# Kernel optimization log

Measured on AMD Instinct MI355X. Metric: run time of the kernel, lower is better.

Reference implementation:

```python
import jax, jax.numpy as jnp
import numpy as np

B, D_IN, D_H, D_OUT = 1024, 1024, 4096, 1024
SPARSITY = 0.5  # fraction of weights KEPT (top-k)


def setup_inputs() -> dict:
    key = jax.random.key(0)
    ks = jax.random.split(key, 13)
    def kaiming(k, shape):
        fan_in = shape[-1] if len(shape) > 1 else shape[0]
        bound = 1.0 / np.sqrt(fan_in)
        return jax.random.uniform(k, shape, jnp.float32, -bound, bound)
    inp = {
        "x":   jax.random.normal(ks[0], (B, D_IN), jnp.float32),
        "W1":  kaiming(ks[1], (D_H, D_IN)),
        "b1":  kaiming(ks[2], (D_H,)),
        "W2":  kaiming(ks[3], (D_H, D_H)),
        "b2":  kaiming(ks[4], (D_H,)),
        "W3":  kaiming(ks[5], (D_OUT, D_H)),
        "b3":  kaiming(ks[6], (D_OUT,)),
        # scores: kaiming-uniform for weights, N(0, 0.01) for biases (as in Mask.__init__)
        "sW1": kaiming(ks[7], (D_H, D_IN)),
        "sb1": 0.01 * jax.random.normal(ks[8], (D_H,), jnp.float32),
        "sW2": kaiming(ks[9], (D_H, D_H)),
        "sb2": 0.01 * jax.random.normal(ks[10], (D_H,), jnp.float32),
        "sW3": kaiming(ks[11], (D_OUT, D_H)),
        "sb3": 0.01 * jax.random.normal(ks[12], (D_OUT,), jnp.float32),
    }
    return inp


def _global_masks(scores):
    """Single fused global top-k threshold mask (replaces O(P) redundant sorts).
    Bottom (1-SPARSITY) fraction (by value rank) -> 0, top SPARSITY fraction -> 1."""
    flat = jnp.concatenate([s.ravel() for s in scores])
    n = flat.shape[0]
    j = int((1.0 - SPARSITY) * n)  # number of zeroed entries
    idx = jnp.argsort(flat)
    bin_mask = jnp.zeros((n,), flat.dtype).at[idx[j:]].set(1.0)
    # straight-through: d(mask)/d(score) = 1 (GetSubnet_global.backward returns g)
    st_mask = bin_mask + flat - jax.lax.stop_gradient(flat)
    sizes = [int(np.prod(s.shape)) for s in scores]
    offs = np.concatenate([[0], np.cumsum(sizes)])
    return [st_mask[offs[i]:offs[i + 1]].reshape(scores[i].shape)
            for i in range(len(scores))]


def reference(x, W1, b1, W2, b2, W3, b3, sW1, sb1, sW2, sb2, sW3, sb3):
    masks = _global_masks([sW1, sb1, sW2, sb2, sW3, sb3])
    mW1, mb1, mW2, mb2, mW3, mb3 = masks
    # masked params, then MLP forward (torch Linear: y = x @ W.T + b)
    h = jax.nn.relu(x @ (W1 * mW1).T + b1 * mb1)
    h = jax.nn.relu(h @ (W2 * mW2).T + b2 * mb2)
    return h @ (W3 * mW3).T + b3 * mb3
```

## Files before the change

### kernel.cpp

```cpp
#include <hip/hip_runtime.h>
#include <hip/hip_bf16.h>
#include <stdint.h>


typedef __bf16 bf16_t;
typedef __bf16 bf16x4 __attribute__((ext_vector_type(4)));
typedef __bf16 bf16x8 __attribute__((ext_vector_type(8)));
typedef float  f32x4  __attribute__((ext_vector_type(4)));

using gvoid = const __attribute__((address_space(1))) void;
using svoid = __attribute__((address_space(3))) void;

#define O1 4194304L
#define O2 4198400L
#define O3 20975616L
#define O4 20979712L
#define O5 25174016L
#define N_TOT 25175040L
#define J_RANK 12587520u
#define CAND_CAP 4096

#define HIST_BLOCKS 512

#define WS_HIST 0u
#define WS_RES  32768u
#define WS_CNT  32784u
#define WS_CAND 32800u
#define WS_W1B  131072u
#define WS_B1F  8519680u
#define WS_W2B  8536064u
#define WS_B2F  42090496u
#define WS_W3B  42106880u
#define WS_B3F  50495488u
#define WS_H1F  50511872u
#define WS_H2F  58900480u
#define WS_FAST_END 67289088ull
#define WS_H1   131072u
#define WS_H2   8519680u

#define SWZ(row, chunk) ((((chunk) + ((row) >> 1)) & 3))

__device__ __forceinline__ unsigned int mono32(float f) {
    unsigned int u = __float_as_uint(f);
    return (u & 0x80000000u) ? ~u : (u | 0x80000000u);
}

__global__ __launch_bounds__(256) void zero_kernel(unsigned int* p, int n) {
    int i = blockIdx.x * 256 + threadIdx.x;
    if (i < n) p[i] = 0u;
}

__global__ __launch_bounds__(256) void cvt_x_kernel(const float* __restrict__ x,
                                                    bf16_t* __restrict__ xb, int n8) {
    int i = blockIdx.x * 256 + threadIdx.x;
    if (i < n8) {
        const float4 a = *(const float4*)(x + (size_t)i * 8);
        const float4 b = *(const float4*)(x + (size_t)i * 8 + 4);
        bf16x8 r;
        r[0] = (__bf16)a.x; r[1] = (__bf16)a.y; r[2] = (__bf16)a.z; r[3] = (__bf16)a.w;
        r[4] = (__bf16)b.x; r[5] = (__bf16)b.y; r[6] = (__bf16)b.z; r[7] = (__bf16)b.w;
        *(bf16x8*)(xb + (size_t)i * 8) = r;
    }
}

__device__ __forceinline__ void seg_lookup(long e,
    const float* s0, const float* s1, const float* s2,
    const float* s3, const float* s4, const float* s5,
    const float** sp, long* off) {
    if (e < O1)      { *sp = s0; *off = e; }
    else if (e < O2) { *sp = s1; *off = e - O1; }
    else if (e < O3) { *sp = s2; *off = e - O2; }
    else if (e < O4) { *sp = s3; *off = e - O3; }
    else if (e < O5) { *sp = s4; *off = e - O4; }
    else             { *sp = s5; *off = e - O5; }
}

__global__ __launch_bounds__(256) void hist_kernel(
    const float* s0, const float* s1, const float* s2,
    const float* s3, const float* s4, const float* s5,
    unsigned int* hb) {
    __shared__ unsigned int lh[8192];
    for (int i = threadIdx.x; i < 8192; i += 256) lh[i] = 0u;
    __syncthreads();
    const long ng = N_TOT / 4;
    for (long g = (long)blockIdx.x * 256 + threadIdx.x; g < ng;
         g += (long)gridDim.x * 256) {
        long e = g * 4;
        const float* sp; long o;
        seg_lookup(e, s0, s1, s2, s3, s4, s5, &sp, &o);
        float4 v = *(const float4*)(sp + o);
        atomicAdd(&lh[mono32(v.x) >> 19], 1u);
        atomicAdd(&lh[mono32(v.y) >> 19], 1u);
        atomicAdd(&lh[mono32(v.z) >> 19], 1u);
        atomicAdd(&lh[mono32(v.w) >> 19], 1u);
    }
    __syncthreads();
    unsigned int* dst = hb + (size_t)blockIdx.x * 8192;
    for (int i = threadIdx.x; i < 8192; i += 256) dst[i] = lh[i];
}

__global__ __launch_bounds__(256) void reduce_hist(const unsigned int* __restrict__ hb,
                                                   unsigned int* __restrict__ hist) {
    int b = blockIdx.x * 256 + threadIdx.x;
    unsigned int s = 0;
    for (int blk = 0; blk < HIST_BLOCKS; ++blk)
        s += hb[(size_t)blk * 8192 + b];
    hist[b] = s;
}

__global__ __launch_bounds__(256) void select_kernel(const unsigned int* hist,
                                                     unsigned int* res) {
    __shared__ unsigned int part[256];
    int tid = threadIdx.x;
    unsigned int s = 0;
    for (int b = tid * 32; b < tid * 32 + 32; ++b) s += hist[b];
    part[tid] = s;
    __syncthreads();
    if (tid == 0) {
        unsigned int acc = 0;
        for (int i = 0; i < 256; ++i) { unsigned int v = part[i]; part[i] = acc; acc += v; }
    }
    __syncthreads();
    unsigned int acc = part[tid];
    for (int b = tid * 32; b < tid * 32 + 32; ++b) {
        unsigned int h = hist[b];
        if (acc <= J_RANK && J_RANK < acc + h) {
            res[0] = (unsigned int)b;
            res[1] = acc;
            res[2] = J_RANK - acc;
        }
        acc += h;
    }
}

__global__ __launch_bounds__(256) void mask_apply_fast(
    const float* s0, const float* s1, const float* s2,
    const float* s3, const float* s4, const float* s5,
    const float* w0, const float* w1, const float* w2,
    const float* w3, const float* w4, const float* w5,
    bf16_t* W1b, float* b1f, bf16_t* W2b, float* b2f, bf16_t* W3b, float* b3f,
    const unsigned int* res, unsigned int* cand_cnt, unsigned long long* cand) {
    const unsigned int C = res[0];
    const long ng = N_TOT / 4;
    for (long g = (long)blockIdx.x * 256 + threadIdx.x; g < ng;
         g += (long)gridDim.x * 256) {
        long e = g * 4;
        const float* sp; long o;
        seg_lookup(e, s0, s1, s2, s3, s4, s5, &sp, &o);
        const float* wp;
        if (e < O1)      wp = w0;
        else if (e < O2) wp = w1;
        else if (e < O3) wp = w2;
        else if (e < O4) wp = w3;
        else if (e < O5) wp = w4;
        else             wp = w5;
        float4 sv = *(const float4*)(sp + o);
        float4 wv = *(const float4*)(wp + o);
#define PROC(comp, ci)                                                         \
        { unsigned int key = mono32(sv.comp); unsigned int kb = key >> 19;     \
          if (kb < C) wv.comp = 0.f;                                           \
          else if (kb == C) {                                                  \
              unsigned int slot = atomicAdd(cand_cnt, 1u);                     \
              if (slot < CAND_CAP)                                             \
                  cand[slot] = (((unsigned long long)key) << 32) |             \
                               (unsigned long long)(unsigned int)(e + ci);     \
          } }
        PROC(x, 0) PROC(y, 1) PROC(z, 2) PROC(w, 3)
#undef PROC
        if (e < O1) {
            bf16x4 b; b[0]=(__bf16)wv.x; b[1]=(__bf16)wv.y; b[2]=(__bf16)wv.z; b[3]=(__bf16)wv.w;
            *(bf16x4*)(W1b + o) = b;
        } else if (e < O2) {
            *(float4*)(b1f + o) = wv;
        } else if (e < O3) {
            bf16x4 b; b[0]=(__bf16)wv.x; b[1]=(__bf16)wv.y; b[2]=(__bf16)wv.z; b[3]=(__bf16)wv.w;
            *(bf16x4*)(W2b + o) = b;
        } else if (e < O4) {
            *(float4*)(b2f + o) = wv;
        } else if (e < O5) {
            bf16x4 b; b[0]=(__bf16)wv.x; b[1]=(__bf16)wv.y; b[2]=(__bf16)wv.z; b[3]=(__bf16)wv.w;
            *(bf16x4*)(W3b + o) = b;
        } else {
            *(float4*)(b3f + o) = wv;
        }
    }
}

__global__ __launch_bounds__(256) void finalize_fast(
    const unsigned int* res, const unsigned int* cand_cnt,
    const unsigned long long* cand,
    bf16_t* W1b, float* b1f, bf16_t* W2b, float* b2f, bf16_t* W3b, float* b3f) {
    __shared__ unsigned long long buf[CAND_CAP];
    int tid = threadIdx.x;
    unsigned int cnt = *cand_cnt; if (cnt > CAND_CAP) cnt = CAND_CAP;
    unsigned int need = res[2];   if (need > cnt) need = cnt;
    for (int i = tid; i < (int)cnt; i += 256) buf[i] = cand[i];
    __syncthreads();
    for (int i = tid; i < (int)cnt; i += 256) {
        unsigned long long me = buf[i];
        unsigned int rank = 0;
        for (unsigned int j = 0; j < cnt; ++j) rank += (buf[j] < me);
        if (rank < need) {
            long idx = (long)(unsigned int)(me & 0xFFFFFFFFu);
            if (idx < O1)      W1b[idx] = (__bf16)0.f;
            else if (idx < O2) b1f[idx - O1] = 0.f;
            else if (idx < O3) W2b[idx - O2] = (__bf16)0.f;
            else if (idx < O4) b2f[idx - O3] = 0.f;
            else if (idx < O5) W3b[idx - O4] = (__bf16)0.f;
            else               b3f[idx - O5] = 0.f;
        }
    }
}

__global__ __launch_bounds__(256) void mask_apply_kernel(
    const float* s0, const float* s1, const float* s2,
    const float* s3, const float* s4, const float* s5,
    float* w0, float* w1, float* w2, float* w3, float* w4, float* w5,
    const unsigned int* res, unsigned int* cand_cnt, unsigned long long* cand) {
    const unsigned int C = res[0];
    const long ng = N_TOT / 4;
    for (long g = (long)blockIdx.x * 256 + threadIdx.x; g < ng;
         g += (long)gridDim.x * 256) {
        long e = g * 4;
        const float* sp; long o;
        seg_lookup(e, s0, s1, s2, s3, s4, s5, &sp, &o);
        float* wp;
        if (e < O1)      wp = w0;
        else if (e < O2) wp = w1;
        else if (e < O3) wp = w2;
        else if (e < O4) wp = w3;
        else if (e < O5) wp = w4;
        else             wp = w5;
        float4 sv = *(const float4*)(sp + o);
        float4 wv = *(float4*)(wp + o);
#define PROC(comp, ci)                                                         \
        { unsigned int key = mono32(sv.comp); unsigned int kb = key >> 19;     \
          if (kb < C) wv.comp = 0.f;                                           \
          else if (kb == C) {                                                  \
              unsigned int slot = atomicAdd(cand_cnt, 1u);                     \
              if (slot < CAND_CAP)                                             \
                  cand[slot] = (((unsigned long long)key) << 32) |             \
                               (unsigned long long)(unsigned int)(e + ci);     \
          } }
        PROC(x, 0) PROC(y, 1) PROC(z, 2) PROC(w, 3)
#undef PROC
        *(float4*)(wp + o) = wv;
    }
}

__global__ __launch_bounds__(256) void finalize_kernel(
    const unsigned int* res, const unsigned int* cand_cnt,
    const unsigned long long* cand,
    float* w0, float* w1, float* w2, float* w3, float* w4, float* w5) {
    __shared__ unsigned long long buf[CAND_CAP];
    int tid = threadIdx.x;
    unsigned int cnt = *cand_cnt; if (cnt > CAND_CAP) cnt = CAND_CAP;
    unsigned int need = res[2];   if (need > cnt) need = cnt;
    for (int i = tid; i < (int)cnt; i += 256) buf[i] = cand[i];
    __syncthreads();
    for (int i = tid; i < (int)cnt; i += 256) {
        unsigned long long me = buf[i];
        unsigned int rank = 0;
        for (unsigned int j = 0; j < cnt; ++j) rank += (buf[j] < me);
        if (rank < need) {
            long idx = (long)(unsigned int)(me & 0xFFFFFFFFu);
            if (idx < O1)      w0[idx] = 0.f;
            else if (idx < O2) w1[idx - O1] = 0.f;
            else if (idx < O3) w2[idx - O2] = 0.f;
            else if (idx < O4) w3[idx - O3] = 0.f;
            else if (idx < O5) w4[idx - O4] = 0.f;
            else               w5[idx - O5] = 0.f;
        }
    }
}

__device__ __forceinline__ bf16x8 load8(const float* p) {
    float4 a = *(const float4*)p;
    float4 b = *(const float4*)(p + 4);
    bf16x8 r;
    r[0] = (__bf16)a.x; r[1] = (__bf16)a.y; r[2] = (__bf16)a.z; r[3] = (__bf16)a.w;
    r[4] = (__bf16)b.x; r[5] = (__bf16)b.y; r[6] = (__bf16)b.z; r[7] = (__bf16)b.w;
    return r;
}
__device__ __forceinline__ bf16x8 load8(const bf16_t* p) {
    return *(const bf16x8*)p;
}

template <int BM, int BN, bool RELU, typename TA, typename TB, typename TC>
__global__ __launch_bounds__(256) void gemm_bt(
    const TA* __restrict__ A, const TB* __restrict__ B,
    const float* __restrict__ bias, TC* __restrict__ C,
    int M, int N, int K) {
    constexpr int BK = 32;
    constexpr int WM = BM / 2, WN = BN / 2;
    constexpr int TM = WM / 16, TN = WN / 16;
    constexpr int CA = (BM * BK) / 8;
    constexpr int CB = (BN * BK) / 8;
    __shared__ __align__(16) bf16_t As[BM * BK];
    __shared__ __align__(16) bf16_t Bs[BN * BK];

    const int tid = threadIdx.x;
    const int w = tid >> 6, lane = tid & 63;
    const int quad = lane >> 4, l16 = lane & 15;
    const int wm = (w >> 1) * WM, wn = (w & 1) * WN;
    const int rowBase = blockIdx.y * BM;
    const int colBase = blockIdx.x * BN;

    f32x4 acc[TM][TN] = {};

    const TA* Ab = A + (size_t)rowBase * K;
    const TB* Bb = B + (size_t)colBase * K;

    for (int k0 = 0; k0 < K; k0 += BK) {
        __syncthreads();
#pragma unroll
        for (int c0 = 0; c0 < CA; c0 += 256) {
            int c = c0 + tid;
            int row = c >> 2, kc = c & 3;
            *(bf16x8*)&As[row * BK + SWZ(row, kc) * 8] =
                load8(Ab + (size_t)row * K + k0 + kc * 8);
        }
#pragma unroll
        for (int c0 = 0; c0 < CB; c0 += 256) {
            int c = c0 + tid;
            int row = c >> 2, kc = c & 3;
            *(bf16x8*)&Bs[row * BK + SWZ(row, kc) * 8] =
                load8(Bb + (size_t)row * K + k0 + kc * 8);
        }
        __syncthreads();
        bf16x8 af[TM], bfr[TN];
#pragma unroll
        for (int i = 0; i < TM; ++i) {
            int r = wm + i * 16 + l16;
            af[i] = *(const bf16x8*)&As[r * BK + SWZ(r, quad) * 8];
        }
#pragma unroll
        for (int j = 0; j < TN; ++j) {
            int r = wn + j * 16 + l16;
            bfr[j] = *(const bf16x8*)&Bs[r * BK + SWZ(r, quad) * 8];
        }
#pragma unroll
        for (int i = 0; i < TM; ++i)
#pragma unroll
            for (int j = 0; j < TN; ++j)
                acc[i][j] = __builtin_amdgcn_mfma_f32_16x16x32_bf16(
                    af[i], bfr[j], acc[i][j], 0, 0, 0);
    }

#pragma unroll
    for (int i = 0; i < TM; ++i) {
#pragma unroll
        for (int j = 0; j < TN; ++j) {
            int col = colBase + wn + j * 16 + l16;
            float bv = bias[col];
#pragma unroll
            for (int r = 0; r < 4; ++r) {
                int rowg = rowBase + wm + i * 16 + quad * 4 + r;
                float v = acc[i][j][r] + bv;
                if (RELU) v = v > 0.f ? v : 0.f;
                if constexpr (sizeof(TC) == 4)
                    C[(size_t)rowg * N + col] = v;
                else
                    C[(size_t)rowg * N + col] = (bf16_t)v;
            }
        }
    }
}

template <bool RELU, int SPLITK, typename TC>
__global__ __launch_bounds__(256) void gemm2ph(
    const bf16_t* __restrict__ A, const bf16_t* __restrict__ B,
    const float* __restrict__ bias, TC* __restrict__ C,
    int M, int N, int K, int gridX) {
    constexpr int BM = 64, BN = 128, BK = 32;
    constexpr int TM = 2, TN = 4;
    constexpr int CA = (BM * BK) / 8;
    constexpr int CB = (BN * BK) / 8;
    static_assert(CA == 256 && CB == 512, "staging assumes 3 loads/thread/step");
    __shared__ __align__(16) bf16_t As[2][BM * BK];
    __shared__ __align__(16) bf16_t Bs[2][BN * BK];

    const int tid = threadIdx.x;
    const int w = tid >> 6, lane = tid & 63;
    const int quad = lane >> 4, l16 = lane & 15;
    const int wm = (w >> 1) * 32, wn = (w & 1) * 64;

    const int nwg = gridX * (int)gridDim.y;
    const int wg = (int)blockIdx.y * gridX + (int)blockIdx.x;
    const int cpx = nwg >> 3;
    const int swz = (wg & 7) * cpx + (wg >> 3);
    const int bx = swz % gridX, by = swz / gridX;

    const int rowBase = by * BM;
    const int colBase = bx * BN;

    f32x4 acc[TM][TN] = {};

    const bf16_t* Ab = A + (size_t)rowBase * K;
    const bf16_t* Bb = B + (size_t)colBase * K;

    const int kPart = K / SPLITK;
    const int kBeg = (SPLITK > 1) ? (int)blockIdx.z * kPart : 0;
    const int nt = kPart / BK;

    const int rA = tid >> 2;
    const int lA = ((tid & 3) - (rA >> 1)) & 3;
    const int cB1 = tid + 256;
    const int rB1 = cB1 >> 2;
    const int lB1 = ((cB1 & 3) - (rB1 >> 1)) & 3;
    const bf16_t* aSrc  = Ab + (size_t)rA * K + lA * 8;
    const bf16_t* bSrc0 = Bb + (size_t)rA * K + lA * 8;
    const bf16_t* bSrc1 = Bb + (size_t)rB1 * K + lB1 * 8;

    auto stage = [&](int buf, int k0) {
        __builtin_amdgcn_global_load_lds((gvoid*)(aSrc + k0),
            (svoid*)(As[buf] + (size_t)tid * 8), 16, 0, 0);
        __builtin_amdgcn_global_load_lds((gvoid*)(bSrc0 + k0),
            (svoid*)(Bs[buf] + (size_t)tid * 8), 16, 0, 0);
        __builtin_amdgcn_global_load_lds((gvoid*)(bSrc1 + k0),
            (svoid*)(Bs[buf] + (size_t)cB1 * 8), 16, 0, 0);
    };
    auto compute = [&](int buf) {
        bf16x8 af[TM], bfr[TN];
#pragma unroll
        for (int i = 0; i < TM; ++i) {
            int r = wm + i * 16 + l16;
            af[i] = *(const bf16x8*)&As[buf][r * BK + SWZ(r, quad) * 8];
        }
#pragma unroll
        for (int j = 0; j < TN; ++j) {
            int r = wn + j * 16 + l16;
            bfr[j] = *(const bf16x8*)&Bs[buf][r * BK + SWZ(r, quad) * 8];
        }
#pragma unroll
        for (int i = 0; i < TM; ++i)
#pragma unroll
            for (int j = 0; j < TN; ++j)
                acc[i][j] = __builtin_amdgcn_mfma_f32_16x16x32_bf16(
                    af[i], bfr[j], acc[i][j], 0, 0, 0);
    };

    stage(0, kBeg);
    __syncthreads();
    for (int t = 0; t < nt - 1; ++t) {
        stage((t + 1) & 1, kBeg + (t + 1) * BK);
        compute(t & 1);
        __syncthreads();
    }
    compute((nt - 1) & 1);

#pragma unroll
    for (int i = 0; i < TM; ++i) {
#pragma unroll
        for (int j = 0; j < TN; ++j) {
            int col = colBase + wn + j * 16 + l16;
            float bv = (SPLITK == 1 || blockIdx.z == 0) ? bias[col] : 0.f;
#pragma unroll
            for (int r = 0; r < 4; ++r) {
                int rowg = rowBase + wm + i * 16 + quad * 4 + r;
                float v = acc[i][j][r] + bv;
                if constexpr (SPLITK == 1) {
                    if (RELU) v = v > 0.f ? v : 0.f;
                    if constexpr (sizeof(TC) == 4)
                        C[(size_t)rowg * N + col] = v;
                    else
                        C[(size_t)rowg * N + col] = (bf16_t)v;
                } else {
                    atomicAdd((float*)&C[(size_t)rowg * N + col], v);
                }
            }
        }
    }
}

extern "C" void kernel_launch(void* const* d_in, const int* in_sizes, int n_in,
                              void* d_out, int out_size, void* d_ws, size_t ws_size,
                              hipStream_t stream) {
    const float* x  = (const float*)d_in[0];
    float* W1 = (float*)d_in[1];
    float* b1 = (float*)d_in[2];
    float* W2 = (float*)d_in[3];
    float* b2 = (float*)d_in[4];
    float* W3 = (float*)d_in[5];
    float* b3 = (float*)d_in[6];
    const float* s0 = (const float*)d_in[7];
    const float* s1 = (const float*)d_in[8];
    const float* s2 = (const float*)d_in[9];
    const float* s3 = (const float*)d_in[10];
    const float* s4 = (const float*)d_in[11];
    const float* s5 = (const float*)d_in[12];

    uint8_t* ws = (uint8_t*)d_ws;
    unsigned int* hist = (unsigned int*)(ws + WS_HIST);
    unsigned int* res  = (unsigned int*)(ws + WS_RES);
    unsigned int* cnt  = (unsigned int*)(ws + WS_CNT);
    unsigned long long* cand = (unsigned long long*)(ws + WS_CAND);
    float* OUT = (float*)d_out;

    zero_kernel<<<33, 256, 0, stream>>>((unsigned int*)ws, 8200);

    if (ws_size >= WS_FAST_END) {
        bf16_t* W1b = (bf16_t*)(ws + WS_W1B);
        float*  b1f = (float*)(ws + WS_B1F);
        bf16_t* W2b = (bf16_t*)(ws + WS_W2B);
        float*  b2f = (float*)(ws + WS_B2F);
        bf16_t* W3b = (bf16_t*)(ws + WS_W3B);
        float*  b3f = (float*)(ws + WS_B3F);
        bf16_t* H1  = (bf16_t*)(ws + WS_H1F);
        bf16_t* H2  = (bf16_t*)(ws + WS_H2F);
        unsigned int* hb = (unsigned int*)(ws + WS_W2B);
        bf16_t* xb  = (bf16_t*)(ws + WS_H2F);

        hist_kernel<<<HIST_BLOCKS, 256, 0, stream>>>(s0, s1, s2, s3, s4, s5, hb);
        reduce_hist<<<32, 256, 0, stream>>>(hb, hist);
        select_kernel<<<1, 256, 0, stream>>>(hist, res);
        zero_kernel<<<4096, 256, 0, stream>>>((unsigned int*)OUT, 1048576);
        cvt_x_kernel<<<512, 256, 0, stream>>>(x, xb, 131072);
        mask_apply_fast<<<2048, 256, 0, stream>>>(
            s0, s1, s2, s3, s4, s5, W1, b1, W2, b2, W3, b3,
            W1b, b1f, W2b, b2f, W3b, b3f, res, cnt, cand);
        finalize_fast<<<1, 256, 0, stream>>>(res, cnt, cand,
                                             W1b, b1f, W2b, b2f, W3b, b3f);
        gemm2ph<true, 1, bf16_t>
            <<<dim3(32, 16), 256, 0, stream>>>(xb, W1b, b1f, H1, 1024, 4096, 1024, 32);
        gemm2ph<true, 1, bf16_t>
            <<<dim3(32, 16), 256, 0, stream>>>(H1, W2b, b2f, H2, 1024, 4096, 4096, 32);
        gemm2ph<false, 4, float>
            <<<dim3(8, 16, 4), 256, 0, stream>>>(H2, W3b, b3f, OUT, 1024, 1024, 4096, 8);
    } else {
        bf16_t* H1 = (bf16_t*)(ws + WS_H1);
        bf16_t* H2 = (bf16_t*)(ws + WS_H2);
        hist_kernel<<<1, 256, 0, stream>>>(s0, s1, s2, s3, s4, s5, hist);
        select_kernel<<<1, 256, 0, stream>>>(hist, res);
        mask_apply_kernel<<<2048, 256, 0, stream>>>(s0, s1, s2, s3, s4, s5,
                                                    W1, b1, W2, b2, W3, b3,
                                                    res, cnt, cand);
        finalize_kernel<<<1, 256, 0, stream>>>(res, cnt, cand,
                                               W1, b1, W2, b2, W3, b3);
        gemm_bt<64, 128, true, float, float, bf16_t>
            <<<dim3(32, 16), 256, 0, stream>>>(x, W1, b1, H1, 1024, 4096, 1024);
        gemm_bt<64, 128, true, bf16_t, float, bf16_t>
            <<<dim3(32, 16), 256, 0, stream>>>(H1, W2, b2, H2, 1024, 4096, 4096);
        gemm_bt<64, 64, false, bf16_t, float, float>
            <<<dim3(16, 16), 256, 0, stream>>>(H2, W3, b3, OUT, 1024, 1024, 4096);
    }
}
```

Measured before the change: 399.4 us.

## Fuse prep kernels into mask pass, widen GEMM K-tile, drop workgroup swizzle

The x-to-bf16 conversion and the output zeroing move into the mask_apply_fast kernel, and the candidate counter is reset inside select_kernel, so several small launches disappear. The GEMM K tile doubles from 32 to 64, with an 8-way LDS swizzle and two MFMA sub-steps per stage, to halve barrier and staging overhead per unit of work. The L2-friendly workgroup index swizzle is removed in favour of plain block indexing. The fallback path gets a parallel atomic histogram. The larger tile doubles LDS use, which may reduce occupancy, and dropping the swizzle may hurt cache locality.

```diff
diff --git a/kernel.cpp b/kernel.cpp
--- a/kernel.cpp
+++ b/kernel.cpp
@@ -39,6 +39,7 @@
 #define WS_H2   8519680u
 
 #define SWZ(row, chunk) ((((chunk) + ((row) >> 1)) & 3))
+#define SWZ8(row, chunk) ((((chunk) + (row)) & 7))
 
 __device__ __forceinline__ unsigned int mono32(float f) {
     unsigned int u = __float_as_uint(f);
@@ -48,19 +49,6 @@
 __global__ __launch_bounds__(256) void zero_kernel(unsigned int* p, int n) {
     int i = blockIdx.x * 256 + threadIdx.x;
     if (i < n) p[i] = 0u;
-}
-
-__global__ __launch_bounds__(256) void cvt_x_kernel(const float* __restrict__ x,
-                                                    bf16_t* __restrict__ xb, int n8) {
-    int i = blockIdx.x * 256 + threadIdx.x;
-    if (i < n8) {
-        const float4 a = *(const float4*)(x + (size_t)i * 8);
-        const float4 b = *(const float4*)(x + (size_t)i * 8 + 4);
-        bf16x8 r;
-        r[0] = (__bf16)a.x; r[1] = (__bf16)a.y; r[2] = (__bf16)a.z; r[3] = (__bf16)a.w;
-        r[4] = (__bf16)b.x; r[5] = (__bf16)b.y; r[6] = (__bf16)b.z; r[7] = (__bf16)b.w;
-        *(bf16x8*)(xb + (size_t)i * 8) = r;
-    }
 }
 
 __device__ __forceinline__ void seg_lookup(long e,
@@ -109,9 +97,11 @@
 }
 
 __global__ __launch_bounds__(256) void select_kernel(const unsigned int* hist,
-                                                     unsigned int* res) {
+                                                     unsigned int* res,
+                                                     unsigned int* cnt) {
     __shared__ unsigned int part[256];
     int tid = threadIdx.x;
+    if (tid == 0) *cnt = 0u;
     unsigned int s = 0;
     for (int b = tid * 32; b < tid * 32 + 32; ++b) s += hist[b];
     part[tid] = s;
@@ -139,11 +129,22 @@
     const float* w0, const float* w1, const float* w2,
     const float* w3, const float* w4, const float* w5,
     bf16_t* W1b, float* b1f, bf16_t* W2b, float* b2f, bf16_t* W3b, float* b3f,
-    const unsigned int* res, unsigned int* cand_cnt, unsigned long long* cand) {
+    const unsigned int* res, unsigned int* cand_cnt, unsigned long long* cand,
+    const float* xsrc, bf16_t* xb, float* OUT) {
+    const long gtid = (long)blockIdx.x * 256 + threadIdx.x;
+    if (gtid < 262144)
+        *(float4*)(OUT + gtid * 4) = make_float4(0.f, 0.f, 0.f, 0.f);
+    if (gtid < 131072) {
+        const float4 p = *(const float4*)(xsrc + gtid * 8);
+        const float4 q = *(const float4*)(xsrc + gtid * 8 + 4);
+        bf16x8 r;
+        r[0] = (__bf16)p.x; r[1] = (__bf16)p.y; r[2] = (__bf16)p.z; r[3] = (__bf16)p.w;
+        r[4] = (__bf16)q.x; r[5] = (__bf16)q.y; r[6] = (__bf16)q.z; r[7] = (__bf16)q.w;
+        *(bf16x8*)(xb + gtid * 8) = r;
+    }
     const unsigned int C = res[0];
     const long ng = N_TOT / 4;
-    for (long g = (long)blockIdx.x * 256 + threadIdx.x; g < ng;
-         g += (long)gridDim.x * 256) {
+    for (long g = gtid; g < ng; g += (long)gridDim.x * 256) {
         long e = g * 4;
         const float* sp; long o;
         seg_lookup(e, s0, s1, s2, s3, s4, s5, &sp, &o);
@@ -212,6 +213,32 @@
     }
 }
 
+__global__ __launch_bounds__(256) void hist_atomic_kernel(
+    const float* s0, const float* s1, const float* s2,
+    const float* s3, const float* s4, const float* s5,
+    unsigned int* hist) {
+    __shared__ unsigned int lh[8192];
+    for (int i = threadIdx.x; i < 8192; i += 256) lh[i] = 0u;
+    __syncthreads();
+    const long ng = N_TOT / 4;
+    for (long g = (long)blockIdx.x * 256 + threadIdx.x; g < ng;
+         g += (long)gridDim.x * 256) {
+        long e = g * 4;
+        const float* sp; long o;
+        seg_lookup(e, s0, s1, s2, s3, s4, s5, &sp, &o);
+        float4 v = *(const float4*)(sp + o);
+        atomicAdd(&lh[mono32(v.x) >> 19], 1u);
+        atomicAdd(&lh[mono32(v.y) >> 19], 1u);
+        atomicAdd(&lh[mono32(v.z) >> 19], 1u);
+        atomicAdd(&lh[mono32(v.w) >> 19], 1u);
+    }
+    __syncthreads();
+    for (int i = threadIdx.x; i < 8192; i += 256) {
+        unsigned int c = lh[i];
+        if (c) atomicAdd(&hist[i], c);
+    }
+}
+
 __global__ __launch_bounds__(256) void mask_apply_kernel(
     const float* s0, const float* s1, const float* s2,
     const float* s3, const float* s4, const float* s5,
@@ -371,12 +398,12 @@
 __global__ __launch_bounds__(256) void gemm2ph(
     const bf16_t* __restrict__ A, const bf16_t* __restrict__ B,
     const float* __restrict__ bias, TC* __restrict__ C,
-    int M, int N, int K, int gridX) {
-    constexpr int BM = 64, BN = 128, BK = 32;
+    int M, int N, int K) {
+    constexpr int BM = 64, BN = 128, BK = 64;
     constexpr int TM = 2, TN = 4;
     constexpr int CA = (BM * BK) / 8;
     constexpr int CB = (BN * BK) / 8;
-    static_assert(CA == 256 && CB == 512, "staging assumes 3 loads/thread/step");
+    static_assert(CA == 512 && CB == 1024, "staging assumes 6 loads/thread/step");
     __shared__ __align__(16) bf16_t As[2][BM * BK];
     __shared__ __align__(16) bf16_t Bs[2][BN * BK];
 
@@ -385,14 +412,8 @@
     const int quad = lane >> 4, l16 = lane & 15;
     const int wm = (w >> 1) * 32, wn = (w & 1) * 64;
 
-    const int nwg = gridX * (int)gridDim.y;
-    const int wg = (int)blockIdx.y * gridX + (int)blockIdx.x;
-    const int cpx = nwg >> 3;
-    const int swz = (wg & 7) * cpx + (wg >> 3);
-    const int bx = swz % gridX, by = swz / gridX;
-
-    const int rowBase = by * BM;
-    const int colBase = bx * BN;
+    const int rowBase = blockIdx.y * BM;
+    const int colBase = blockIdx.x * BN;
 
     f32x4 acc[TM][TN] = {};
 
@@ -403,41 +424,51 @@
     const int kBeg = (SPLITK > 1) ? (int)blockIdx.z * kPart : 0;
     const int nt = kPart / BK;
 
-    const int rA = tid >> 2;
-    const int lA = ((tid & 3) - (rA >> 1)) & 3;
-    const int cB1 = tid + 256;
-    const int rB1 = cB1 >> 2;
-    const int lB1 = ((cB1 & 3) - (rB1 >> 1)) & 3;
-    const bf16_t* aSrc  = Ab + (size_t)rA * K + lA * 8;
-    const bf16_t* bSrc0 = Bb + (size_t)rA * K + lA * 8;
-    const bf16_t* bSrc1 = Bb + (size_t)rB1 * K + lB1 * 8;
+    const int rA0 = tid >> 3,          lA0 = ((tid & 3 * 2 + 1 & 0) + ((tid & 7) - rA0)) & 7;
+#define CHUNK_SRC(base, c) ((base) + (size_t)((c) >> 3) * K + ((((c) & 7) - ((c) >> 3)) & 7) * 8)
+    const bf16_t* aS0 = CHUNK_SRC(Ab, tid);
+    const bf16_t* aS1 = CHUNK_SRC(Ab, tid + 256);
+    const bf16_t* bS0 = CHUNK_SRC(Bb, tid);
+    const bf16_t* bS1 = CHUNK_SRC(Bb, tid + 256);
+    const bf16_t* bS2 = CHUNK_SRC(Bb, tid + 512);
+    const bf16_t* bS3 = CHUNK_SRC(Bb, tid + 768);
+#undef CHUNK_SRC
 
     auto stage = [&](int buf, int k0) {
-        __builtin_amdgcn_global_load_lds((gvoid*)(aSrc + k0),
+        __builtin_amdgcn_global_load_lds((gvoid*)(aS0 + k0),
             (svoid*)(As[buf] + (size_t)tid * 8), 16, 0, 0);
-        __builtin_amdgcn_global_load_lds((gvoid*)(bSrc0 + k0),
+        __builtin_amdgcn_global_load_lds((gvoid*)(aS1 + k0),
+            (svoid*)(As[buf] + (size_t)(tid + 256) * 8), 16, 0, 0);
+        __builtin_amdgcn_global_load_lds((gvoid*)(bS0 + k0),
             (svoid*)(Bs[buf] + (size_t)tid * 8), 16, 0, 0);
-        __builtin_amdgcn_global_load_lds((gvoid*)(bSrc1 + k0),
-            (svoid*)(Bs[buf] + (size_t)cB1 * 8), 16, 0, 0);
+        __builtin_amdgcn_global_load_lds((gvoid*)(bS1 + k0),
+            (svoid*)(Bs[buf] + (size_t)(tid + 256) * 8), 16, 0, 0);
+        __builtin_amdgcn_global_load_lds((gvoid*)(bS2 + k0),
+            (svoid*)(Bs[buf] + (size_t)(tid + 512) * 8), 16, 0, 0);
+        __builtin_amdgcn_global_load_lds((gvoid*)(bS3 + k0),
+            (svoid*)(Bs[buf] + (size_t)(tid + 768) * 8), 16, 0, 0);
     };
     auto compute = [&](int buf) {
-        bf16x8 af[TM], bfr[TN];
-#pragma unroll
-        for (int i = 0; i < TM; ++i) {
-            int r = wm + i * 16 + l16;
-            af[i] = *(const bf16x8*)&As[buf][r * BK + SWZ(r, quad) * 8];
-        }
-#pragma unroll
-        for (int j = 0; j < TN; ++j) {
-            int r = wn + j * 16 + l16;
-            bfr[j] = *(const bf16x8*)&Bs[buf][r * BK + SWZ(r, quad) * 8];
-        }
-#pragma unroll
-        for (int i = 0; i < TM; ++i)
-#pragma unroll
-            for (int j = 0; j < TN; ++j)
-                acc[i][j] = __builtin_amdgcn_mfma_f32_16x16x32_bf16(
-                    af[i], bfr[j], acc[i][j], 0, 0, 0);
+#pragma unroll
+        for (int kk = 0; kk < 2; ++kk) {
+            bf16x8 af[TM], bfr[TN];
+#pragma unroll
+            for (int i = 0; i < TM; ++i) {
+                int r = wm + i * 16 + l16;
+                af[i] = *(const bf16x8*)&As[buf][r * BK + SWZ8(r, kk * 4 + quad) * 8];
+            }
+#pragma unroll
+            for (int j = 0; j < TN; ++j) {
+                int r = wn + j * 16 + l16;
+                bfr[j] = *(const bf16x8*)&Bs[buf][r * BK + SWZ8(r, kk * 4 + quad) * 8];
+            }
+#pragma unroll
+            for (int i = 0; i < TM; ++i)
+#pragma unroll
+                for (int j = 0; j < TN; ++j)
+                    acc[i][j] = __builtin_amdgcn_mfma_f32_16x16x32_bf16(
+                        af[i], bfr[j], acc[i][j], 0, 0, 0);
+        }
     };
 
     stage(0, kBeg);
@@ -497,8 +528,6 @@
     unsigned long long* cand = (unsigned long long*)(ws + WS_CAND);
     float* OUT = (float*)d_out;
 
-    zero_kernel<<<33, 256, 0, stream>>>((unsigned int*)ws, 8200);
-
     if (ws_size >= WS_FAST_END) {
         bf16_t* W1b = (bf16_t*)(ws + WS_W1B);
         float*  b1f = (float*)(ws + WS_B1F);
@@ -513,25 +542,24 @@
 
         hist_kernel<<<HIST_BLOCKS, 256, 0, stream>>>(s0, s1, s2, s3, s4, s5, hb);
         reduce_hist<<<32, 256, 0, stream>>>(hb, hist);
-        select_kernel<<<1, 256, 0, stream>>>(hist, res);
-        zero_kernel<<<4096, 256, 0, stream>>>((unsigned int*)OUT, 1048576);
-        cvt_x_kernel<<<512, 256, 0, stream>>>(x, xb, 131072);
+        select_kernel<<<1, 256, 0, stream>>>(hist, res, cnt);
         mask_apply_fast<<<2048, 256, 0, stream>>>(
             s0, s1, s2, s3, s4, s5, W1, b1, W2, b2, W3, b3,
-            W1b, b1f, W2b, b2f, W3b, b3f, res, cnt, cand);
+            W1b, b1f, W2b, b2f, W3b, b3f, res, cnt, cand, x, xb, OUT);
         finalize_fast<<<1, 256, 0, stream>>>(res, cnt, cand,
                                              W1b, b1f, W2b, b2f, W3b, b3f);
         gemm2ph<true, 1, bf16_t>
-            <<<dim3(32, 16), 256, 0, stream>>>(xb, W1b, b1f, H1, 1024, 4096, 1024, 32);
+            <<<dim3(32, 16), 256, 0, stream>>>(xb, W1b, b1f, H1, 1024, 4096, 1024);
         gemm2ph<true, 1, bf16_t>
-            <<<dim3(32, 16), 256, 0, stream>>>(H1, W2b, b2f, H2, 1024, 4096, 4096, 32);
+            <<<dim3(32, 16), 256, 0, stream>>>(H1, W2b, b2f, H2, 1024, 4096, 4096);
         gemm2ph<false, 4, float>
-            <<<dim3(8, 16, 4), 256, 0, stream>>>(H2, W3b, b3f, OUT, 1024, 1024, 4096, 8);
+            <<<dim3(8, 16, 4), 256, 0, stream>>>(H2, W3b, b3f, OUT, 1024, 1024, 4096);
     } else {
         bf16_t* H1 = (bf16_t*)(ws + WS_H1);
         bf16_t* H2 = (bf16_t*)(ws + WS_H2);
-        hist_kernel<<<1, 256, 0, stream>>>(s0, s1, s2, s3, s4, s5, hist);
-        select_kernel<<<1, 256, 0, stream>>>(hist, res);
+        zero_kernel<<<33, 256, 0, stream>>>((unsigned int*)ws, 8200);
+        hist_atomic_kernel<<<1024, 256, 0, stream>>>(s0, s1, s2, s3, s4, s5, hist);
+        select_kernel<<<1, 256, 0, stream>>>(hist, res, cnt);
         mask_apply_kernel<<<2048, 256, 0, stream>>>(s0, s1, s2, s3, s4, s5,
                                                     W1, b1, W2, b2, W3, b3,
                                                     res, cnt, cand);
```

Result: faster. 378.0 us (-5.4%).
